# Performance work log

Measured on AMD Instinct MI355X. Metric: run time of the kernel, lower is better.

## Reference

```python
import jax, jax.numpy as jnp
import numpy as np

B, N, K, T, H = 4, 1024, 100, 2, 64
NFEAT = 96  # ntypes * m1 * m2 = 2 * 12 * 4


def setup_inputs() -> dict:
    key = jax.random.key(0)
    ks = jax.random.split(key, 8)
    feat = jax.random.normal(ks[0], (B, N, NFEAT), jnp.float32)
    dfeat = jax.random.normal(ks[1], (B, N, K, NFEAT, 3), jnp.float32) * 0.1
    ImageDR = jax.random.uniform(ks[2], (B, N, K, 4), jnp.float32)
    # 1-based neighbor indices; 0 marks an empty (padded) neighbor slot
    list_neigh_alltype = jax.random.randint(ks[3], (B, N, K), 0, N + 1).astype(jnp.int32)
    Imagetype_map = jnp.sort(jax.random.randint(ks[4], (N,), 0, T)).astype(jnp.int32)
    # per-type FittingNet params: 96 -> 64 -> 64 (resnet w/ resnet_dt) -> 1
    W1 = jax.random.normal(ks[5], (T, NFEAT, H), jnp.float32) * (1.0 / np.sqrt(NFEAT))
    b1 = jnp.zeros((T, H), jnp.float32)
    W2 = jax.random.normal(ks[6], (T, H, H), jnp.float32) * (1.0 / np.sqrt(H))
    b2 = jnp.zeros((T, H), jnp.float32)
    rdt = jnp.full((T, H), 0.1, jnp.float32)  # resnet_dt timestep params
    Wout = jax.random.normal(ks[7], (T, H), jnp.float32) * (1.0 / np.sqrt(H))
    bout = jnp.array([-3.2, -5.1], jnp.float32)  # per-type energy shift
    return dict(feat=feat, dfeat=dfeat, ImageDR=ImageDR,
                list_neigh_alltype=list_neigh_alltype, Imagetype_map=Imagetype_map,
                W1=W1, b1=b1, W2=W2, b2=b2, rdt=rdt, Wout=Wout, bout=bout, nghost=0)


def _fitting_Ei(feat, Imagetype_map, W1, b1, W2, b2, rdt, Wout, bout):
    # Evaluate every per-type fitting net on all atoms, then select by atom type.
    h1 = jnp.tanh(jnp.einsum('bnf,tfh->tbnh', feat, W1) + b1[:, None, None, :])
    h2 = h1 + rdt[:, None, None, :] * jnp.tanh(
        jnp.einsum('tbnh,thg->tbng', h1, W2) + b2[:, None, None, :])
    e = jnp.einsum('tbnh,th->tbn', h2, Wout) + bout[:, None, None]  # (T,B,N)
    sel = Imagetype_map.astype(jnp.int32)[None, :, None]            # (1,N,1)
    Ei = jnp.take_along_axis(e.transpose(1, 2, 0), sel, axis=2)[..., 0]  # (B,N)
    return Ei


def reference(feat, dfeat, ImageDR, list_neigh_alltype, Imagetype_map,
              W1, b1, W2, b2, rdt, Wout, bout, nghost):
    # Ei and dE/dfeat (the torch code uses autograd.grad on Ei wrt feat)
    Ei, vjp_fn = jax.vjp(
        lambda f: _fitting_Ei(f, Imagetype_map, W1, b1, W2, b2, rdt, Wout, bout), feat)
    Etot = Ei.sum(axis=1)                                    # (B,)
    dE = vjp_fn(jnp.ones_like(Ei))[0]                        # (B,N,NFEAT)
    # dE_dfeat[b,i,k,:] = sum_f dE[b,i,f] * dfeat[b,i,k,f,:]
    dE_dfeat = jnp.einsum('bnf,bnkfx->bnkx', dE, dfeat)      # (B,N,K,3)
    valid = (list_neigh_alltype > 0).astype(dE_dfeat.dtype)[..., None]
    pair_f = dE_dfeat * valid
    # force buffer sized natoms + nghost + 1; slot 0 absorbs padded neighbors
    Fbuf = jnp.zeros((B, N + 1 + nghost, 3), dE_dfeat.dtype)
    bidx = jnp.arange(B)[:, None, None]
    Fbuf = Fbuf.at[bidx, list_neigh_alltype].add(pair_f)     # scatter to neighbors
    Fbuf = Fbuf.at[:, 1:N + 1, :].add(-pair_f.sum(axis=2))   # center-atom reaction
    Force = Fbuf[:, 1:N + 1, :]                              # (B,N,3)
    rij = ImageDR[..., 1:4]                                  # (B,N,K,3)
    Virial = -jnp.einsum('bnkx,bnky->bxy', rij, pair_f).reshape(B, 9)
    return Etot, Ei, Force, Virial
```

## Files before the change

### kernel.cpp

```cpp
#include <hip/hip_runtime.h>

#define BB 4
#define NN 1024
#define KK 100
#define TT 2
#define HH 64
#define FF 96
#define KPW 25

#define OFF_EI   4
#define OFF_F    (4 + BB*NN)
#define OFF_VIR  (OFF_F + BB*NN*3)
#define OUT_TOT  (OFF_VIR + BB*9)

#define WS_W1T   0
#define WS_W2T   (TT*HH*FF)
#define PREP_MAX ((OUT_TOT > TT*FF*HH) ? OUT_TOT : TT*FF*HH)

__device__ __forceinline__ float wave_sum(float v) {
    #pragma unroll
    for (int off = 32; off > 0; off >>= 1)
        v += __shfl_xor(v, off, 64);
    return v;
}

__global__ __launch_bounds__(256) void prep_kernel(
    const float* __restrict__ W1, const float* __restrict__ W2,
    float* __restrict__ ws, float* __restrict__ out)
{
    int i = blockIdx.x * 256 + threadIdx.x;
    if (i < OUT_TOT) out[i] = 0.f;
    float* W1T = ws + WS_W1T;
    float* W2T = ws + WS_W2T;
    if (i < TT * FF * HH) {
        int t = i / (FF * HH), r = i % (FF * HH);
        int f = r / HH, h = r % HH;
        W1T[(t * HH + h) * FF + f] = W1[i];
    }
    if (i < TT * HH * HH) {
        int t = i / (HH * HH), r = i % (HH * HH);
        int h = r / HH, g = r % HH;
        W2T[(t * HH + g) * HH + h] = W2[i];
    }
}

__global__ __launch_bounds__(256) void fused_kernel(
    const float* __restrict__ feat, const int* __restrict__ tmap,
    const float* __restrict__ W1, const float* __restrict__ b1,
    const float* __restrict__ W2, const float* __restrict__ b2,
    const float* __restrict__ rdt, const float* __restrict__ Wout,
    const float* __restrict__ bout, const float* __restrict__ ws,
    const float* __restrict__ dfeat, const float* __restrict__ ImageDR,
    const int* __restrict__ neigh, float* __restrict__ out)
{
    const int row  = blockIdx.x;
    const int b    = row / NN;
    const int n    = row - b * NN;
    const int tid  = threadIdx.x;
    const int wave = tid >> 6;
    const int lane = tid & 63;
    const int k0   = wave * KPW;

    __shared__ float sdr[KK * 4];
    __shared__ int   snb[KK];

    {
        const float* drbase = ImageDR + (size_t)row * (KK * 4);
        for (int i = lane; i < KPW * 4; i += 64)
            sdr[k0 * 4 + i] = drbase[k0 * 4 + i];
        if (lane < KPW)
            snb[k0 + lane] = neigh[(size_t)row * KK + k0 + lane];
    }

    const int t = tmap[n];
    const float* frow = feat + (size_t)row * FF;
    const float* W1t  = W1 + (size_t)t * FF * HH;
    const float* W2t  = W2 + (size_t)t * HH * HH;
    const float* W1Tt = ws + WS_W1T + (size_t)t * HH * FF;
    const float* W2Tt = ws + WS_W2T + (size_t)t * HH * HH;

    float f0 = frow[lane];
    float f1 = (lane < 32) ? frow[HH + lane] : 0.f;

    float z1 = b1[t * HH + lane];
    #pragma unroll 8
    for (int f = 0; f < HH; ++f)
        z1 = fmaf(__shfl(f0, f, 64), W1t[f * HH + lane], z1);
    #pragma unroll 8
    for (int f = 0; f < FF - HH; ++f)
        z1 = fmaf(__shfl(f1, f, 64), W1t[(HH + f) * HH + lane], z1);
    float h1 = tanhf(z1);

    float z2 = b2[t * HH + lane];
    #pragma unroll 8
    for (int h = 0; h < HH; ++h)
        z2 = fmaf(__shfl(h1, h, 64), W2t[h * HH + lane], z2);
    float u  = tanhf(z2);
    float r  = rdt[t * HH + lane];
    float wo = Wout[t * HH + lane];

    float e = wave_sum((h1 + r * u) * wo);

    float dz2 = r * wo * (1.f - u * u);
    float dh1 = wo;
    #pragma unroll 8
    for (int g = 0; g < HH; ++g)
        dh1 = fmaf(__shfl(dz2, g, 64), W2Tt[g * HH + lane], dh1);
    float dz1 = dh1 * (1.f - h1 * h1);

    float w0 = 0.f, w1 = 0.f;
    #pragma unroll 8
    for (int h = 0; h < HH; ++h) {
        const float d = __shfl(dz1, h, 64);
        w0 = fmaf(d, W1Tt[h * FF + lane], w0);
        if (lane < 32) w1 = fmaf(d, W1Tt[h * FF + HH + lane], w1);
    }

    if (wave == 0 && lane == 0) {
        const float Ei = e + bout[t];
        out[OFF_EI + row] = Ei;
        atomicAdd(&out[b], Ei);
    }

    float sacc0 = 0.f, sacc1 = 0.f, sacc2 = 0.f;
    float vacc  = 0.f;
    const int vx = lane / 3, vy = lane - 3 * vx;

    const size_t pbase = (size_t)row * KK;

    #pragma unroll 2
    for (int k = k0; k < k0 + KPW; ++k) {
        const float* dfp = dfeat + (pbase + k) * (FF * 3);
        float a0 = dfp[lane * 3 + 0] * w0;
        float a1 = dfp[lane * 3 + 1] * w0;
        float a2 = dfp[lane * 3 + 2] * w0;
        if (lane < 32) {
            const int m = (HH + lane) * 3;
            a0 = fmaf(dfp[m + 0], w1, a0);
            a1 = fmaf(dfp[m + 1], w1, a1);
            a2 = fmaf(dfp[m + 2], w1, a2);
        }
        float pf0 = wave_sum(a0);
        float pf1 = wave_sum(a1);
        float pf2 = wave_sum(a2);

        const int j = snb[k];
        if (j <= 0) { pf0 = 0.f; pf1 = 0.f; pf2 = 0.f; }
        else if (lane < 3) {
            const float v = (lane == 0) ? pf0 : ((lane == 1) ? pf1 : pf2);
            atomicAdd(&out[OFF_F + ((size_t)b * NN + (j - 1)) * 3 + lane], v);
        }

        sacc0 -= pf0; sacc1 -= pf1; sacc2 -= pf2;

        if (lane < 9) {
            const float rx  = sdr[k * 4 + 1 + vx];
            const float pfy = (vy == 0) ? pf0 : ((vy == 1) ? pf1 : pf2);
            vacc = fmaf(-rx, pfy, vacc);
        }
    }

    if (lane < 3) {
        const float s = (lane == 0) ? sacc0 : ((lane == 1) ? sacc1 : sacc2);
        atomicAdd(&out[OFF_F + (size_t)row * 3 + lane], s);
    }
    if (lane < 9) atomicAdd(&out[OFF_VIR + b * 9 + lane], vacc);
}

extern "C" void kernel_launch(void* const* d_in, const int* in_sizes, int n_in,
                              void* d_out, int out_size, void* d_ws, size_t ws_size,
                              hipStream_t stream) {
    const float* feat    = (const float*)d_in[0];
    const float* dfeat   = (const float*)d_in[1];
    const float* ImageDR = (const float*)d_in[2];
    const int*   neigh   = (const int*)  d_in[3];
    const int*   tmap    = (const int*)  d_in[4];
    const float* W1      = (const float*)d_in[5];
    const float* b1      = (const float*)d_in[6];
    const float* W2      = (const float*)d_in[7];
    const float* b2      = (const float*)d_in[8];
    const float* rdt     = (const float*)d_in[9];
    const float* Wout    = (const float*)d_in[10];
    const float* bout    = (const float*)d_in[11];

    float* out = (float*)d_out;
    float* ws  = (float*)d_ws;

    prep_kernel<<<(PREP_MAX + 255) / 256, 256, 0, stream>>>(W1, W2, ws, out);
    fused_kernel<<<BB * NN, 256, 0, stream>>>(feat, tmap, W1, b1, W2, b2, rdt,
                                              Wout, bout, ws, dfeat, ImageDR,
                                              neigh, out);
}
```

Measured before the change: 879.1 us.

## Assign one atom per wave and split neighbor dot products across 4-lane groups

```diff
diff --git a/kernel.cpp b/kernel.cpp
--- a/kernel.cpp
+++ b/kernel.cpp
@@ -6,7 +6,6 @@
 #define TT 2
 #define HH 64
 #define FF 96
-#define KPW 25
 
 #define OFF_EI   4
 #define OFF_F    (4 + BB*NN)
@@ -16,6 +15,8 @@
 #define WS_W1T   0
 #define WS_W2T   (TT*HH*FF)
 #define PREP_MAX ((OUT_TOT > TT*FF*HH) ? OUT_TOT : TT*FF*HH)
+
+#define NPASS    ((KK + 15) / 16)
 
 __device__ __forceinline__ float wave_sum(float v) {
     #pragma unroll
@@ -53,118 +54,142 @@
     const float* __restrict__ dfeat, const float* __restrict__ ImageDR,
     const int* __restrict__ neigh, float* __restrict__ out)
 {
-    const int row  = blockIdx.x;
-    const int b    = row / NN;
-    const int n    = row - b * NN;
     const int tid  = threadIdx.x;
     const int wave = tid >> 6;
     const int lane = tid & 63;
-    const int k0   = wave * KPW;
-
-    __shared__ float sdr[KK * 4];
-    __shared__ int   snb[KK];
+    const int row  = blockIdx.x * 4 + wave;
+    const int b    = row >> 10;
+    const int n    = row & (NN - 1);
+
+    __shared__ float sdE[4][FF];
 
     {
-        const float* drbase = ImageDR + (size_t)row * (KK * 4);
-        for (int i = lane; i < KPW * 4; i += 64)
-            sdr[k0 * 4 + i] = drbase[k0 * 4 + i];
-        if (lane < KPW)
-            snb[k0 + lane] = neigh[(size_t)row * KK + k0 + lane];
-    }
-
-    const int t = tmap[n];
-    const float* frow = feat + (size_t)row * FF;
-    const float* W1t  = W1 + (size_t)t * FF * HH;
-    const float* W2t  = W2 + (size_t)t * HH * HH;
-    const float* W1Tt = ws + WS_W1T + (size_t)t * HH * FF;
-    const float* W2Tt = ws + WS_W2T + (size_t)t * HH * HH;
-
-    float f0 = frow[lane];
-    float f1 = (lane < 32) ? frow[HH + lane] : 0.f;
-
-    float z1 = b1[t * HH + lane];
-    #pragma unroll 8
-    for (int f = 0; f < HH; ++f)
-        z1 = fmaf(__shfl(f0, f, 64), W1t[f * HH + lane], z1);
-    #pragma unroll 8
-    for (int f = 0; f < FF - HH; ++f)
-        z1 = fmaf(__shfl(f1, f, 64), W1t[(HH + f) * HH + lane], z1);
-    float h1 = tanhf(z1);
-
-    float z2 = b2[t * HH + lane];
-    #pragma unroll 8
-    for (int h = 0; h < HH; ++h)
-        z2 = fmaf(__shfl(h1, h, 64), W2t[h * HH + lane], z2);
-    float u  = tanhf(z2);
-    float r  = rdt[t * HH + lane];
-    float wo = Wout[t * HH + lane];
-
-    float e = wave_sum((h1 + r * u) * wo);
-
-    float dz2 = r * wo * (1.f - u * u);
-    float dh1 = wo;
-    #pragma unroll 8
-    for (int g = 0; g < HH; ++g)
-        dh1 = fmaf(__shfl(dz2, g, 64), W2Tt[g * HH + lane], dh1);
-    float dz1 = dh1 * (1.f - h1 * h1);
-
-    float w0 = 0.f, w1 = 0.f;
-    #pragma unroll 8
-    for (int h = 0; h < HH; ++h) {
-        const float d = __shfl(dz1, h, 64);
-        w0 = fmaf(d, W1Tt[h * FF + lane], w0);
-        if (lane < 32) w1 = fmaf(d, W1Tt[h * FF + HH + lane], w1);
-    }
-
-    if (wave == 0 && lane == 0) {
-        const float Ei = e + bout[t];
-        out[OFF_EI + row] = Ei;
-        atomicAdd(&out[b], Ei);
-    }
-
-    float sacc0 = 0.f, sacc1 = 0.f, sacc2 = 0.f;
-    float vacc  = 0.f;
-    const int vx = lane / 3, vy = lane - 3 * vx;
-
-    const size_t pbase = (size_t)row * KK;
-
-    #pragma unroll 2
-    for (int k = k0; k < k0 + KPW; ++k) {
-        const float* dfp = dfeat + (pbase + k) * (FF * 3);
-        float a0 = dfp[lane * 3 + 0] * w0;
-        float a1 = dfp[lane * 3 + 1] * w0;
-        float a2 = dfp[lane * 3 + 2] * w0;
-        if (lane < 32) {
-            const int m = (HH + lane) * 3;
-            a0 = fmaf(dfp[m + 0], w1, a0);
-            a1 = fmaf(dfp[m + 1], w1, a1);
-            a2 = fmaf(dfp[m + 2], w1, a2);
-        }
-        float pf0 = wave_sum(a0);
-        float pf1 = wave_sum(a1);
-        float pf2 = wave_sum(a2);
-
-        const int j = snb[k];
-        if (j <= 0) { pf0 = 0.f; pf1 = 0.f; pf2 = 0.f; }
-        else if (lane < 3) {
-            const float v = (lane == 0) ? pf0 : ((lane == 1) ? pf1 : pf2);
-            atomicAdd(&out[OFF_F + ((size_t)b * NN + (j - 1)) * 3 + lane], v);
-        }
-
-        sacc0 -= pf0; sacc1 -= pf1; sacc2 -= pf2;
-
-        if (lane < 9) {
-            const float rx  = sdr[k * 4 + 1 + vx];
-            const float pfy = (vy == 0) ? pf0 : ((vy == 1) ? pf1 : pf2);
-            vacc = fmaf(-rx, pfy, vacc);
-        }
-    }
-
-    if (lane < 3) {
-        const float s = (lane == 0) ? sacc0 : ((lane == 1) ? sacc1 : sacc2);
-        atomicAdd(&out[OFF_F + (size_t)row * 3 + lane], s);
-    }
-    if (lane < 9) atomicAdd(&out[OFF_VIR + b * 9 + lane], vacc);
+        const int t = tmap[n];
+        const float* frow = feat + (size_t)row * FF;
+        const float* W1t  = W1 + (size_t)t * FF * HH;
+        const float* W2t  = W2 + (size_t)t * HH * HH;
+        const float* W1Tt = ws + WS_W1T + (size_t)t * HH * FF;
+        const float* W2Tt = ws + WS_W2T + (size_t)t * HH * HH;
+
+        float f0 = frow[lane];
+        float f1 = (lane < 32) ? frow[HH + lane] : 0.f;
+
+        float z1 = b1[t * HH + lane];
+        #pragma unroll 8
+        for (int f = 0; f < HH; ++f)
+            z1 = fmaf(__shfl(f0, f, 64), W1t[f * HH + lane], z1);
+        #pragma unroll 8
+        for (int f = 0; f < FF - HH; ++f)
+            z1 = fmaf(__shfl(f1, f, 64), W1t[(HH + f) * HH + lane], z1);
+        float h1 = tanhf(z1);
+
+        float z2 = b2[t * HH + lane];
+        #pragma unroll 8
+        for (int h = 0; h < HH; ++h)
+            z2 = fmaf(__shfl(h1, h, 64), W2t[h * HH + lane], z2);
+        float u  = tanhf(z2);
+        float r  = rdt[t * HH + lane];
+        float wo = Wout[t * HH + lane];
+
+        float e = wave_sum((h1 + r * u) * wo);
+
+        float dz2 = r * wo * (1.f - u * u);
+        float dh1 = wo;
+        #pragma unroll 8
+        for (int g = 0; g < HH; ++g)
+            dh1 = fmaf(__shfl(dz2, g, 64), W2Tt[g * HH + lane], dh1);
+        float dz1 = dh1 * (1.f - h1 * h1);
+
+        float w0 = 0.f, w1 = 0.f;
+        #pragma unroll 8
+        for (int h = 0; h < HH; ++h) {
+            const float d = __shfl(dz1, h, 64);
+            w0 = fmaf(d, W1Tt[h * FF + lane], w0);
+            if (lane < 32) w1 = fmaf(d, W1Tt[h * FF + HH + lane], w1);
+        }
+
+        sdE[wave][lane] = w0;
+        if (lane < 32) sdE[wave][HH + lane] = w1;
+
+        if (lane == 0) {
+            const float Ei = e + bout[t];
+            out[OFF_EI + row] = Ei;
+            atomicAdd(&out[b], Ei);
+        }
+    }
+    __syncthreads();
+
+    const int g = lane >> 2;
+    const int q = lane & 3;
+    const float* sd = sdE[wave];
+    const size_t rowPair = (size_t)row * KK;
+
+    int jv[NPASS];
+    #pragma unroll
+    for (int p = 0; p < NPASS; ++p) {
+        const int k = p * 16 + g;
+        jv[p] = (k < KK) ? neigh[rowPair + k] : 0;
+    }
+
+    float ssum0 = 0.f, ssum1 = 0.f, ssum2 = 0.f;
+    float vir[9] = {0.f,0.f,0.f,0.f,0.f,0.f,0.f,0.f,0.f};
+
+    for (int p = 0; p < NPASS; ++p) {
+        const int k = p * 16 + g;
+        const bool act = (k < KK);
+        float a0 = 0.f, a1 = 0.f, a2 = 0.f;
+        if (act) {
+            const float* dfp = dfeat + (rowPair + k) * (FF * 3);
+            #pragma unroll
+            for (int it = 0; it < FF / 4; ++it) {
+                const int f = it * 4 + q;
+                const float d = sd[f];
+                const float3 v = *(const float3*)(dfp + f * 3);
+                a0 = fmaf(v.x, d, a0);
+                a1 = fmaf(v.y, d, a1);
+                a2 = fmaf(v.z, d, a2);
+            }
+        }
+        a0 += __shfl_xor(a0, 1, 64); a0 += __shfl_xor(a0, 2, 64);
+        a1 += __shfl_xor(a1, 1, 64); a1 += __shfl_xor(a1, 2, 64);
+        a2 += __shfl_xor(a2, 1, 64); a2 += __shfl_xor(a2, 2, 64);
+
+        if (act && q == 0) {
+            const int j = jv[p];
+            if (j > 0) {
+                const float* drp = ImageDR + (rowPair + k) * 4;
+                const float rx = drp[1], ry = drp[2], rz = drp[3];
+                atomicAdd(&out[OFF_F + ((size_t)b * NN + (j - 1)) * 3 + 0], a0);
+                atomicAdd(&out[OFF_F + ((size_t)b * NN + (j - 1)) * 3 + 1], a1);
+                atomicAdd(&out[OFF_F + ((size_t)b * NN + (j - 1)) * 3 + 2], a2);
+                ssum0 += a0; ssum1 += a1; ssum2 += a2;
+                vir[0] = fmaf(rx, a0, vir[0]);
+                vir[1] = fmaf(rx, a1, vir[1]);
+                vir[2] = fmaf(rx, a2, vir[2]);
+                vir[3] = fmaf(ry, a0, vir[3]);
+                vir[4] = fmaf(ry, a1, vir[4]);
+                vir[5] = fmaf(ry, a2, vir[5]);
+                vir[6] = fmaf(rz, a0, vir[6]);
+                vir[7] = fmaf(rz, a1, vir[7]);
+                vir[8] = fmaf(rz, a2, vir[8]);
+            }
+        }
+    }
+
+    const float S0 = wave_sum(ssum0);
+    const float S1 = wave_sum(ssum1);
+    const float S2 = wave_sum(ssum2);
+    #pragma unroll
+    for (int i = 0; i < 9; ++i) vir[i] = wave_sum(vir[i]);
+
+    if (lane == 0) {
+        atomicAdd(&out[OFF_F + (size_t)row * 3 + 0], -S0);
+        atomicAdd(&out[OFF_F + (size_t)row * 3 + 1], -S1);
+        atomicAdd(&out[OFF_F + (size_t)row * 3 + 2], -S2);
+        #pragma unroll
+        for (int i = 0; i < 9; ++i)
+            atomicAdd(&out[OFF_VIR + b * 9 + i], -vir[i]);
+    }
 }
 
 extern "C" void kernel_launch(void* const* d_in, const int* in_sizes, int n_in,
@@ -187,7 +212,7 @@
     float* ws  = (float*)d_ws;
 
     prep_kernel<<<(PREP_MAX + 255) / 256, 256, 0, stream>>>(W1, W2, ws, out);
-    fused_kernel<<<BB * NN, 256, 0, stream>>>(feat, tmap, W1, b1, W2, b2, rdt,
-                                              Wout, bout, ws, dfeat, ImageDR,
-                                              neigh, out);
-}
+    fused_kernel<<<BB * NN / 4, 256, 0, stream>>>(feat, tmap, W1, b1, W2, b2,
+                                                  rdt, Wout, bout, ws, dfeat,
+                                                  ImageDR, neigh, out);
+}
```

Result: slower. 992.1 us (+12.8%).
